# Kernel tuning notes

Hardware: AMD Instinct MI355X
Metric: run time of the kernel (lower is better)

Reference implementation:

```python
import math
import jax, jax.numpy as jnp
import numpy as np

B, H, T, D = 1, 4, 1024, 8192  # D = 128 * 256 // 4 (hardcoded module constants)
THETA = 2.0 ** 16


def _frequency(d):
    # quantize(arange(d)) = floor(t/2)*2 ; freq = 1/theta**(q/d)/(2*pi)
    t = jnp.arange(d, dtype=jnp.float32)
    q = jnp.floor(t / 2.0) * 2.0
    return 1.0 / (THETA ** (q / d)) / (2.0 * math.pi)  # [D]


def _rope(v):
    # Faithful to original: slices dim 1 (heads), then row-major reshape back.
    v_rot = jnp.stack([-v[:, 1::2], v[:, ::2]], axis=-1).reshape(v.shape)
    freq = _frequency(v.shape[-1])  # [D]
    phases = jnp.arange(v.shape[2], dtype=jnp.float32)[:, None] * freq[None, :]  # [T, D]
    phases = (phases % 1.0) * (2.0 * math.pi)
    cos = jnp.cos(phases)[None, None]  # [1,1,T,D]
    sin = jnp.sin(phases)[None, None]
    return (v * cos).astype(v.dtype) + (v_rot * sin).astype(v.dtype)


def setup_inputs() -> dict:
    key = jax.random.key(0)
    k1, k2 = jax.random.split(key)
    query = jax.random.normal(k1, (B, H, T, D), dtype=jnp.float32)
    value = jax.random.normal(k2, (B, H, T, D), dtype=jnp.float32)
    return {"query": query, "value": value}


def reference(query, value):
    # key is query (asserted in original)
    q = _rope(query)  # [B,H,T,D]
    scale = 1.0 / math.sqrt(D)
    scores = jnp.einsum('bhtd,bhsd->bhts', q, q) * scale  # [B,H,T,T]
    t_idx = jnp.arange(T)
    causal = t_idx[:, None] > t_idx[None, :]  # tril(diagonal=-1): strictly lower
    scores = jnp.where(causal[None, None], scores, 0.0)
    return jnp.einsum('bhts,bhsd->bhtd', scores, value)
```

## Files before the change

### kernel.cpp

```cpp
#include <hip/hip_runtime.h>
#include <hip/hip_bf16.h>


typedef __bf16 bf16x8 __attribute__((ext_vector_type(8)));
typedef float  f32x4  __attribute__((ext_vector_type(4)));

#define HEAD_STRIDE (1024ull * 8192ull)

__device__ inline void gl_lds16(const void* g, void* l) {
  __builtin_amdgcn_global_load_lds(
      (__attribute__((address_space(1))) void*)(g),
      (__attribute__((address_space(3))) void*)(l), 16, 0, 0);
}

__global__ __launch_bounds__(256) void rope_kernel(const float* __restrict__ Q,
                                                   __bf16* __restrict__ Qr) {
  int gid = blockIdx.x * 256 + threadIdx.x;
  size_t e8 = (size_t)gid * 8;
  int d0 = (int)(e8 & 8191);
  int t  = (int)((e8 >> 13) & 1023);
  int h  = (int)(e8 >> 23);

  f32x4 qa = *(const f32x4*)(Q + e8);
  f32x4 qb = *(const f32x4*)(Q + e8 + 4);
  int pt   = t & 1;
  int srct = ((h & 1) << 9) + (t >> 1);
  int sd   = (d0 >> 1) + (pt << 12);
  int hh   = h & ~1;
  size_t soff = ((size_t)srct << 13) + (size_t)sd;
  f32x4 a4 = *(const f32x4*)(Q + (size_t)(hh + 1) * HEAD_STRIDE + soff);
  f32x4 b4 = *(const f32x4*)(Q + (size_t)hh       * HEAD_STRIDE + soff);

  float qv[8];
#pragma unroll
  for (int i = 0; i < 4; ++i) { qv[i] = qa[i]; qv[4 + i] = qb[i]; }

  bf16x8 o;
  float tf = (float)t;
#pragma unroll
  for (int p = 0; p < 4; ++p) {
    float qd = (float)(d0 + 2 * p);
    float fr = exp2f(-qd * (1.0f / 512.0f)) * 0.15915494309189535f;
    float x = tf * fr;
    x -= floorf(x);
    float sn, cs;
    __sincosf(x * 6.283185307179586f, &sn, &cs);
    o[2 * p]     = (__bf16)(qv[2 * p]     * cs - a4[p] * sn);
    o[2 * p + 1] = (__bf16)(qv[2 * p + 1] * cs + b4[p] * sn);
  }
  *(bf16x8*)(Qr + e8) = o;
}

__global__ __launch_bounds__(256) void s1_qqt(const __bf16* __restrict__ Qr,
                                              __bf16* __restrict__ Sbf,
                                              __bf16* __restrict__ part) {
  __shared__ __align__(16) __bf16 As[2][128 * 64];
  __shared__ __align__(16) __bf16 Bs[2][128 * 64];
  int bid = blockIdx.x;
  int x = bid & 7;
  int g = bid >> 3;
  int hi = (g >= 36) ? 1 : 0;
  int pair = g - 36 * hi;
  int c = x * 2 + hi;
  int h = c >> 2, split = c & 3;
  int ti = 0, p = pair;
  while (p > ti) { p -= ti + 1; ++ti; }
  int si = p;

  const __bf16* Abase = Qr + (size_t)h * HEAD_STRIDE + ((size_t)(ti * 128) << 13) + split * 2048;
  const __bf16* Bbase = Qr + (size_t)h * HEAD_STRIDE + ((size_t)(si * 128) << 13) + split * 2048;

  int tid = threadIdx.x, lane = tid & 63, wave = tid >> 6;
  int wm = (wave & 1) << 6, wn = (wave >> 1) << 6;
  int l16 = lane & 15, q4 = lane >> 4;
  int srow = lane >> 3;
  int scol = ((lane & 7) ^ srow) * 8;

  auto stage = [&](int b, int kk) {
#pragma unroll
    for (int j = 0; j < 4; ++j) {
      int cc = wave * 4 + j;
      int row = cc * 8 + srow;
      gl_lds16(Abase + (size_t)row * 8192 + kk + scol, &As[b][cc * 512]);
      gl_lds16(Bbase + (size_t)row * 8192 + kk + scol, &Bs[b][cc * 512]);
    }
  };

  f32x4 acc[4][4] = {};

  stage(0, 0);
  __syncthreads();

  int cur = 0;
  for (int kk = 0; kk < 2048; kk += 64) {
    if (kk + 64 < 2048) stage(cur ^ 1, kk + 64);
#pragma unroll
    for (int ks = 0; ks < 64; ks += 32) {
      bf16x8 af[4], bfr[4];
#pragma unroll
      for (int i = 0; i < 4; ++i) {
        int r = wm + i * 16 + l16;
        af[i] = *(const bf16x8*)&As[cur][r * 64 + (((q4 + (ks >> 3)) ^ (r & 7)) << 3)];
      }
#pragma unroll
      for (int i = 0; i < 4; ++i) {
        int r = wn + i * 16 + l16;
        bfr[i] = *(const bf16x8*)&Bs[cur][r * 64 + (((q4 + (ks >> 3)) ^ (r & 7)) << 3)];
      }
#pragma unroll
      for (int i = 0; i < 4; ++i)
#pragma unroll
        for (int j = 0; j < 4; ++j)
          acc[i][j] = __builtin_amdgcn_mfma_f32_16x16x32_bf16(af[i], bfr[j], acc[i][j], 0, 0, 0);
    }
    __syncthreads();
    cur ^= 1;
  }

  const float scale = 0.011048543456039806f;
  if (split == 0) {
    __bf16* Sh = Sbf + ((size_t)h << 20);
    int t_base = ti * 128 + wm, s_base = si * 128 + wn;
#pragma unroll
    for (int i = 0; i < 4; ++i)
#pragma unroll
      for (int j = 0; j < 4; ++j) {
        int col = s_base + j * 16 + l16;
#pragma unroll
        for (int r = 0; r < 4; ++r) {
          int row = t_base + i * 16 + q4 * 4 + r;
          Sh[((size_t)row << 10) + col] = (__bf16)(acc[i][j][r] * scale);
        }
      }
  } else {
    __bf16* P = part + (((size_t)(h * 36 + pair) * 3 + (split - 1)) << 14);
#pragma unroll
    for (int i = 0; i < 4; ++i)
#pragma unroll
      for (int j = 0; j < 4; ++j) {
        int lcol = wn + j * 16 + l16;
#pragma unroll
        for (int r = 0; r < 4; ++r) {
          int lrow = wm + i * 16 + q4 * 4 + r;
          P[lrow * 128 + lcol] = (__bf16)(acc[i][j][r] * scale);
        }
      }
  }
}

__global__ __launch_bounds__(256) void reduce_kernel(const __bf16* __restrict__ part,
                                                     __bf16* __restrict__ Sbf) {
  int gid = blockIdx.x * 256 + threadIdx.x;
  int tile = gid >> 11;
  int e = (gid & 2047) << 3;
  int row = e >> 7, col = e & 127;
  int h = tile / 36, pair = tile % 36;
  int ti = 0, p = pair;
  while (p > ti) { p -= ti + 1; ++ti; }
  int si = p;

  size_t soff = ((size_t)h << 20) + ((size_t)(ti * 128 + row) << 10) + si * 128 + col;
  bf16x8 s0 = *(const bf16x8*)(Sbf + soff);
  const __bf16* P = part + ((size_t)tile * 3 << 14) + row * 128 + col;
  bf16x8 p0 = *(const bf16x8*)(P);
  bf16x8 p1 = *(const bf16x8*)(P + 16384);
  bf16x8 p2 = *(const bf16x8*)(P + 32768);
  bool diag = (ti == si);
  bf16x8 o;
#pragma unroll
  for (int j = 0; j < 8; ++j) {
    float v = (float)s0[j] + (float)p0[j] + (float)p1[j] + (float)p2[j];
    if (diag && (col + j >= row)) v = 0.0f;
    o[j] = (__bf16)v;
  }
  *(bf16x8*)(Sbf + soff) = o;
}

__global__ __launch_bounds__(256) void transp_kernel(const float* __restrict__ V,
                                                     __bf16* __restrict__ Vt) {
  __shared__ __bf16 L[64 * 72];
  int bid = blockIdx.x;
  int dtile = bid & 127;
  int st = (bid >> 7) & 15;
  int h = bid >> 11;
  int s0 = st << 6, d0 = dtile << 6;
  const float* Vh = V + (size_t)h * HEAD_STRIDE;
  __bf16* Vth = Vt + (size_t)h * HEAD_STRIDE;
  int tid = threadIdx.x;
  int r = tid >> 2;
  int c = (tid & 3) << 4;
#pragma unroll
  for (int j = 0; j < 4; ++j) {
    f32x4 v = *(const f32x4*)(Vh + (size_t)(s0 + r) * 8192 + d0 + c + 4 * j);
#pragma unroll
    for (int e = 0; e < 4; ++e) L[(c + 4 * j + e) * 72 + r] = (__bf16)v[e];
  }
  __syncthreads();
  int row = tid >> 3;
  int col8 = (tid & 7) << 3;
#pragma unroll
  for (int half = 0; half < 2; ++half) {
    int dr = row + half * 32;
    bf16x8 v = *(const bf16x8*)&L[dr * 72 + col8];
    *(bf16x8*)(Vth + (size_t)(d0 + dr) * 1024 + s0 + col8) = v;
  }
}

__global__ __launch_bounds__(256) void s3_sv(const __bf16* __restrict__ Sbf,
                                             const __bf16* __restrict__ Vt,
                                             float* __restrict__ out) {
  __shared__ __align__(16) __bf16 As[2][128 * 64];
  __shared__ __align__(16) __bf16 Bs[2][128 * 64];
  int bid = blockIdx.x;
  int dt = bid & 63; bid >>= 6;
  int tt = 7 - (bid & 7);
  int h = bid >> 3;

  const __bf16* Abase = Sbf + ((size_t)h << 20) + ((size_t)(tt * 128) << 10);
  const __bf16* Bbase = Vt + (size_t)h * HEAD_STRIDE + ((size_t)(dt * 128) << 10);
  int Kmax = tt * 128 + 128;

  int tid = threadIdx.x, lane = tid & 63, wave = tid >> 6;
  int wm = (wave & 1) << 6, wn = (wave >> 1) << 6;
  int l16 = lane & 15, q4 = lane >> 4;
  int srow = lane >> 3;
  int scol = ((lane & 7) ^ srow) * 8;

  auto stage = [&](int b, int kk) {
#pragma unroll
    for (int j = 0; j < 4; ++j) {
      int cc = wave * 4 + j;
      int row = cc * 8 + srow;
      gl_lds16(Abase + (size_t)row * 1024 + kk + scol, &As[b][cc * 512]);
      gl_lds16(Bbase + (size_t)row * 1024 + kk + scol, &Bs[b][cc * 512]);
    }
  };

  f32x4 acc[4][4] = {};

  stage(0, 0);
  __syncthreads();

  int cur = 0;
  for (int kk = 0; kk < Kmax; kk += 64) {
    if (kk + 64 < Kmax) stage(cur ^ 1, kk + 64);
#pragma unroll
    for (int ks = 0; ks < 64; ks += 32) {
      bf16x8 af[4], bfr[4];
#pragma unroll
      for (int i = 0; i < 4; ++i) {
        int r = wm + i * 16 + l16;
        af[i] = *(const bf16x8*)&As[cur][r * 64 + (((q4 + (ks >> 3)) ^ (r & 7)) << 3)];
      }
#pragma unroll
      for (int i = 0; i < 4; ++i) {
        int r = wn + i * 16 + l16;
        bfr[i] = *(const bf16x8*)&Bs[cur][r * 64 + (((q4 + (ks >> 3)) ^ (r & 7)) << 3)];
      }
#pragma unroll
      for (int i = 0; i < 4; ++i)
#pragma unroll
        for (int j = 0; j < 4; ++j)
          acc[i][j] = __builtin_amdgcn_mfma_f32_16x16x32_bf16(af[i], bfr[j], acc[i][j], 0, 0, 0);
    }
    __syncthreads();
    cur ^= 1;
  }

  int t_base = tt * 128 + wm, d_base = dt * 128 + wn;
  float* obase = out + (size_t)h * HEAD_STRIDE;
#pragma unroll
  for (int i = 0; i < 4; ++i)
#pragma unroll
    for (int j = 0; j < 4; ++j) {
      int col = d_base + j * 16 + l16;
#pragma unroll
      for (int r = 0; r < 4; ++r) {
        int row = t_base + i * 16 + q4 * 4 + r;
        obase[((size_t)row << 13) + col] = acc[i][j][r];
      }
    }
}

extern "C" void kernel_launch(void* const* d_in, const int* in_sizes, int n_in,
                              void* d_out, int out_size, void* d_ws, size_t ws_size,
                              hipStream_t stream) {
  const float* query = (const float*)d_in[0];
  const float* value = (const float*)d_in[1];
  float* out = (float*)d_out;

  char* ws = (char*)d_ws;
  __bf16* Qr   = (__bf16*)ws;
  __bf16* Vt   = (__bf16*)ws;
  __bf16* Sbf  = (__bf16*)(ws + 67108864);
  __bf16* part = (__bf16*)(ws + 75497472);

  hipMemsetAsync(Sbf, 0, 8388608, stream);
  rope_kernel<<<16384, 256, 0, stream>>>(query, Qr);
  s1_qqt<<<576, 256, 0, stream>>>(Qr, Sbf, part);
  reduce_kernel<<<1152, 256, 0, stream>>>(part, Sbf);
  transp_kernel<<<8192, 256, 0, stream>>>(value, Vt);
  s3_sv<<<2048, 256, 0, stream>>>(Sbf, Vt, out);
}
```

Before: 446.0 us.

## Widen S·V tile to 128x256 and drop LDS double buffering

The S·V GEMM kernel now computes a 128x256 output tile per block, so each loaded S tile is reused across two V tiles and the grid halves to 1024 blocks. Double buffering is removed: each K step loads single-buffered A and a 2x128 B tile, then syncs before compute. Block ordering also changes to iterate heads and d-tiles inside each t-tile, so the heaviest causal rows are scheduled first. Accumulator registers double (128 floats), which may lower occupancy, and without prefetch the loads no longer overlap the MFMA work.

```diff
diff --git a/kernel.cpp b/kernel.cpp
--- a/kernel.cpp
+++ b/kernel.cpp
@@ -209,15 +209,16 @@
 __global__ __launch_bounds__(256) void s3_sv(const __bf16* __restrict__ Sbf,
                                              const __bf16* __restrict__ Vt,
                                              float* __restrict__ out) {
-  __shared__ __align__(16) __bf16 As[2][128 * 64];
+  __shared__ __align__(16) __bf16 As[128 * 64];
   __shared__ __align__(16) __bf16 Bs[2][128 * 64];
   int bid = blockIdx.x;
-  int dt = bid & 63; bid >>= 6;
-  int tt = 7 - (bid & 7);
-  int h = bid >> 3;
+  int tt = 7 - (bid >> 7);
+  int r2 = bid & 127;
+  int h = r2 >> 5;
+  int dtp = r2 & 31;
 
   const __bf16* Abase = Sbf + ((size_t)h << 20) + ((size_t)(tt * 128) << 10);
-  const __bf16* Bbase = Vt + (size_t)h * HEAD_STRIDE + ((size_t)(dt * 128) << 10);
+  const __bf16* Bbase = Vt + (size_t)h * HEAD_STRIDE + ((size_t)(dtp * 256) << 10);
   int Kmax = tt * 128 + 128;
 
   int tid = threadIdx.x, lane = tid & 63, wave = tid >> 6;
@@ -226,60 +227,64 @@
   int srow = lane >> 3;
   int scol = ((lane & 7) ^ srow) * 8;
 
-  auto stage = [&](int b, int kk) {
+  f32x4 acc[2][4][4] = {};
+
+  for (int kk = 0; kk < Kmax; kk += 64) {
 #pragma unroll
     for (int j = 0; j < 4; ++j) {
       int cc = wave * 4 + j;
       int row = cc * 8 + srow;
-      gl_lds16(Abase + (size_t)row * 1024 + kk + scol, &As[b][cc * 512]);
-      gl_lds16(Bbase + (size_t)row * 1024 + kk + scol, &Bs[b][cc * 512]);
-    }
-  };
-
-  f32x4 acc[4][4] = {};
-
-  stage(0, 0);
-  __syncthreads();
-
-  int cur = 0;
-  for (int kk = 0; kk < Kmax; kk += 64) {
-    if (kk + 64 < Kmax) stage(cur ^ 1, kk + 64);
+      gl_lds16(Abase + (size_t)row * 1024 + kk + scol, &As[cc * 512]);
+    }
+#pragma unroll
+    for (int j = 0; j < 8; ++j) {
+      int cc = wave * 8 + j;
+      int bt = cc >> 4, rc = cc & 15;
+      int row = rc * 8 + srow;
+      gl_lds16(Bbase + (size_t)(bt * 128 + row) * 1024 + kk + scol, &Bs[bt][rc * 512]);
+    }
+    __syncthreads();
 #pragma unroll
     for (int ks = 0; ks < 64; ks += 32) {
-      bf16x8 af[4], bfr[4];
+      bf16x8 af[4];
 #pragma unroll
       for (int i = 0; i < 4; ++i) {
         int r = wm + i * 16 + l16;
-        af[i] = *(const bf16x8*)&As[cur][r * 64 + (((q4 + (ks >> 3)) ^ (r & 7)) << 3)];
-      }
-#pragma unroll
-      for (int i = 0; i < 4; ++i) {
-        int r = wn + i * 16 + l16;
-        bfr[i] = *(const bf16x8*)&Bs[cur][r * 64 + (((q4 + (ks >> 3)) ^ (r & 7)) << 3)];
-      }
-#pragma unroll
-      for (int i = 0; i < 4; ++i)
-#pragma unroll
-        for (int j = 0; j < 4; ++j)
-          acc[i][j] = __builtin_amdgcn_mfma_f32_16x16x32_bf16(af[i], bfr[j], acc[i][j], 0, 0, 0);
+        af[i] = *(const bf16x8*)&As[r * 64 + (((q4 + (ks >> 3)) ^ (r & 7)) << 3)];
+      }
+#pragma unroll
+      for (int bt = 0; bt < 2; ++bt) {
+        bf16x8 bfr[4];
+#pragma unroll
+        for (int i = 0; i < 4; ++i) {
+          int r = wn + i * 16 + l16;
+          bfr[i] = *(const bf16x8*)&Bs[bt][r * 64 + (((q4 + (ks >> 3)) ^ (r & 7)) << 3)];
+        }
+#pragma unroll
+        for (int i = 0; i < 4; ++i)
+#pragma unroll
+          for (int j = 0; j < 4; ++j)
+            acc[bt][i][j] = __builtin_amdgcn_mfma_f32_16x16x32_bf16(af[i], bfr[j], acc[bt][i][j], 0, 0, 0);
+      }
     }
     __syncthreads();
-    cur ^= 1;
-  }
-
-  int t_base = tt * 128 + wm, d_base = dt * 128 + wn;
+  }
+
+  int t_base = tt * 128 + wm;
   float* obase = out + (size_t)h * HEAD_STRIDE;
 #pragma unroll
-  for (int i = 0; i < 4; ++i)
-#pragma unroll
-    for (int j = 0; j < 4; ++j) {
-      int col = d_base + j * 16 + l16;
-#pragma unroll
-      for (int r = 0; r < 4; ++r) {
-        int row = t_base + i * 16 + q4 * 4 + r;
-        obase[((size_t)row << 13) + col] = acc[i][j][r];
-      }
-    }
+  for (int bt = 0; bt < 2; ++bt)
+#pragma unroll
+    for (int i = 0; i < 4; ++i)
+#pragma unroll
+      for (int j = 0; j < 4; ++j) {
+        int col = dtp * 256 + bt * 128 + wn + j * 16 + l16;
+#pragma unroll
+        for (int r = 0; r < 4; ++r) {
+          int row = t_base + i * 16 + q4 * 4 + r;
+          obase[((size_t)row << 13) + col] = acc[bt][i][j][r];
+        }
+      }
 }
 
 extern "C" void kernel_launch(void* const* d_in, const int* in_sizes, int n_in,
@@ -300,5 +305,5 @@
   s1_qqt<<<576, 256, 0, stream>>>(Qr, Sbf, part);
   reduce_kernel<<<1152, 256, 0, stream>>>(part, Sbf);
   transp_kernel<<<8192, 256, 0, stream>>>(value, Vt);
-  s3_sv<<<2048, 256, 0, stream>>>(Sbf, Vt, out);
-}
+  s3_sv<<<1024, 256, 0, stream>>>(Sbf, Vt, out);
+}
```

New measurement: 464.6 us. 1.04x slower.

## Load MFMA fragments directly from global memory in S@V kernel, dropping LDS staging

Applied to the files above, without the earlier changes.

The S@V GEMM kernel no longer stages A and B tiles through double-buffered LDS with global_load_lds and barriers. Each wave now reads its bf16x8 MFMA fragments straight from global memory in a 32-wide K loop. This removes LDS traffic and __syncthreads. In exchange, tiles shared across waves are fetched repeatedly through the caches, and there is no explicit prefetch to hide load latency.

```diff
diff --git a/kernel.cpp b/kernel.cpp
--- a/kernel.cpp
+++ b/kernel.cpp
@@ -209,62 +209,40 @@
 __global__ __launch_bounds__(256) void s3_sv(const __bf16* __restrict__ Sbf,
                                              const __bf16* __restrict__ Vt,
                                              float* __restrict__ out) {
-  __shared__ __align__(16) __bf16 As[2][128 * 64];
-  __shared__ __align__(16) __bf16 Bs[2][128 * 64];
   int bid = blockIdx.x;
   int dt = bid & 63; bid >>= 6;
   int tt = 7 - (bid & 7);
   int h = bid >> 3;
 
-  const __bf16* Abase = Sbf + ((size_t)h << 20) + ((size_t)(tt * 128) << 10);
-  const __bf16* Bbase = Vt + (size_t)h * HEAD_STRIDE + ((size_t)(dt * 128) << 10);
   int Kmax = tt * 128 + 128;
 
   int tid = threadIdx.x, lane = tid & 63, wave = tid >> 6;
   int wm = (wave & 1) << 6, wn = (wave >> 1) << 6;
   int l16 = lane & 15, q4 = lane >> 4;
-  int srow = lane >> 3;
-  int scol = ((lane & 7) ^ srow) * 8;
-
-  auto stage = [&](int b, int kk) {
-#pragma unroll
-    for (int j = 0; j < 4; ++j) {
-      int cc = wave * 4 + j;
-      int row = cc * 8 + srow;
-      gl_lds16(Abase + (size_t)row * 1024 + kk + scol, &As[b][cc * 512]);
-      gl_lds16(Bbase + (size_t)row * 1024 + kk + scol, &Bs[b][cc * 512]);
-    }
-  };
+
+  const __bf16* Ap[4];
+  const __bf16* Bp[4];
+  const __bf16* Abase = Sbf + ((size_t)h << 20) + ((size_t)(tt * 128) << 10) + q4 * 8;
+  const __bf16* Bbase = Vt + (size_t)h * HEAD_STRIDE + ((size_t)(dt * 128) << 10) + q4 * 8;
+#pragma unroll
+  for (int i = 0; i < 4; ++i) {
+    Ap[i] = Abase + (size_t)(wm + i * 16 + l16) * 1024;
+    Bp[i] = Bbase + (size_t)(wn + i * 16 + l16) * 1024;
+  }
 
   f32x4 acc[4][4] = {};
 
-  stage(0, 0);
-  __syncthreads();
-
-  int cur = 0;
-  for (int kk = 0; kk < Kmax; kk += 64) {
-    if (kk + 64 < Kmax) stage(cur ^ 1, kk + 64);
-#pragma unroll
-    for (int ks = 0; ks < 64; ks += 32) {
-      bf16x8 af[4], bfr[4];
-#pragma unroll
-      for (int i = 0; i < 4; ++i) {
-        int r = wm + i * 16 + l16;
-        af[i] = *(const bf16x8*)&As[cur][r * 64 + (((q4 + (ks >> 3)) ^ (r & 7)) << 3)];
-      }
-#pragma unroll
-      for (int i = 0; i < 4; ++i) {
-        int r = wn + i * 16 + l16;
-        bfr[i] = *(const bf16x8*)&Bs[cur][r * 64 + (((q4 + (ks >> 3)) ^ (r & 7)) << 3)];
-      }
-#pragma unroll
-      for (int i = 0; i < 4; ++i)
-#pragma unroll
-        for (int j = 0; j < 4; ++j)
-          acc[i][j] = __builtin_amdgcn_mfma_f32_16x16x32_bf16(af[i], bfr[j], acc[i][j], 0, 0, 0);
-    }
-    __syncthreads();
-    cur ^= 1;
+  for (int kk = 0; kk < Kmax; kk += 32) {
+    bf16x8 af[4], bfr[4];
+#pragma unroll
+    for (int i = 0; i < 4; ++i) af[i]  = *(const bf16x8*)(Ap[i] + kk);
+#pragma unroll
+    for (int i = 0; i < 4; ++i) bfr[i] = *(const bf16x8*)(Bp[i] + kk);
+#pragma unroll
+    for (int i = 0; i < 4; ++i)
+#pragma unroll
+      for (int j = 0; j < 4; ++j)
+        acc[i][j] = __builtin_amdgcn_mfma_f32_16x16x32_bf16(af[i], bfr[j], acc[i][j], 0, 0, 0);
   }
 
   int t_base = tt * 128 + wm, d_base = dt * 128 + wn;
```

Measured after the change: 526.7 us. 1.18x slower.
